# Kernel tuning notes

Measured on AMD Instinct MI355X. Metric: run time of the kernel, lower is better.

Reference implementation:

```python
import jax, jax.numpy as jnp
import numpy as np
from jax import lax

B, C_IN, C_OUT, KK, KS = 8, 32, 64, 4, 3
D, H, W = 32, 64, 64
PAD = 1

def setup_inputs() -> dict:
    key = jax.random.key(0)
    ks = jax.random.split(key, 12)
    s = 0.02
    return {
        "x": jax.random.normal(ks[0], (B, C_IN, D, H, W), jnp.float32),
        # K candidate conv kernels and biases
        "weight": jax.random.normal(ks[1], (KK, C_OUT, C_IN, KS, KS, KS), jnp.float32) * s,
        "cbias": jnp.zeros((KK, C_OUT), jnp.float32),
        "temperature": jnp.float32(34.0),
        # attention key path: BN(affine, eval-mode) -> GELU -> 1x1 conv (linear)
        "bn1_g": jnp.ones((C_IN,), jnp.float32),
        "bn1_b": jnp.zeros((C_IN,), jnp.float32),
        "w1": jax.random.normal(ks[2], (C_IN, C_IN), jnp.float32) * s,
        "b1": jnp.zeros((C_IN,), jnp.float32),
        "bn2_g": jnp.ones((C_IN,), jnp.float32),
        "bn2_b": jnp.zeros((C_IN,), jnp.float32),
        "w2": jax.random.normal(ks[3], (C_IN, C_IN), jnp.float32) * s,
        "b2": jnp.zeros((C_IN,), jnp.float32),
        "bn3_g": jnp.ones((C_IN,), jnp.float32),
        "bn3_b": jnp.zeros((C_IN,), jnp.float32),
        "w3": jax.random.normal(ks[4], (KK, C_IN), jnp.float32) * s,
        "b3": jnp.zeros((KK,), jnp.float32),
    }

def _attention(p, temperature, bn1_g, bn1_b, w1, b1, bn2_g, bn2_b, w2, b2, bn3_g, bn3_b, w3, b3):
    # p: [B, C] pooled features. 1x1x1 convs on 1x1x1 maps == linear layers.
    gelu = lambda t: jax.nn.gelu(t, approximate=False)  # torch nn.GELU default is erf
    a = gelu(p * bn1_g + bn1_b)          # BN (eval: rm=0, rv=1) + GELU
    a = a @ w1.T + b1
    a = gelu(a * bn2_g + bn2_b)
    a = a @ w2.T + b2
    a = a + p                            # ResidualLayer (plain add)
    a = a * bn3_g + bn3_b
    logits = a @ w3.T + b3               # [B, K]
    return jax.nn.softmax(logits / temperature, axis=1)

def reference(x, weight, cbias, temperature, bn1_g, bn1_b, w1, b1,
              bn2_g, bn2_b, w2, b2, bn3_g, bn3_b, w3, b3):
    # x: [B, C_in, D, H, W]
    p = x.mean(axis=(2, 3, 4))  # AdaptiveAvgPool3d(1)
    attn = _attention(p, temperature, bn1_g, bn1_b, w1, b1,
                      bn2_g, bn2_b, w2, b2, bn3_g, bn3_b, w3, b3)  # [B, K]
    # per-sample aggregated kernels / bias
    agg_w = jnp.einsum('bk,koidhw->boidhw', attn, weight)  # [B, O, I, k, k, k]
    agg_b = attn @ cbias                                    # [B, O]
    # grouped-conv trick (groups=B) == per-sample conv3d -> vmap over batch
    def conv1(xi, wi):
        return lax.conv_general_dilated(
            xi[None], wi, window_strides=(1, 1, 1),
            padding=[(PAD, PAD)] * 3,
            dimension_numbers=('NCDHW', 'OIDHW', 'NCDHW'))[0]
    out = jax.vmap(conv1)(x, agg_w)  # [B, O, D, H, W]
    return out + agg_b[:, :, None, None, None]
```

## Files before the change

### kernel.cpp

```cpp
#include <hip/hip_runtime.h>
#include <hip/hip_bf16.h>
#include <math.h>

#define B_   8
#define CIN  32
#define COUT 64
#define KK_  4
#define DD   32
#define HH   64
#define WW   64
#define HW   (HH*WW)
#define DHW  (DD*HH*WW)

typedef __attribute__((ext_vector_type(8)))  short bf16x8;
typedef __attribute__((ext_vector_type(16))) float f32x16;

__device__ __forceinline__ unsigned short f2bf(float f) {
    union { float f; unsigned int u; } v; v.f = f;
    return (unsigned short)((v.u + 0x7FFFu + ((v.u >> 16) & 1u)) >> 16);
}
__device__ __forceinline__ void gll16(const void* g, void* l) {
    __builtin_amdgcn_global_load_lds(
        (const __attribute__((address_space(1))) void*)g,
        (__attribute__((address_space(3))) void*)l, 16, 0, 0);
}

__global__ __launch_bounds__(256) void transpose_kernel(const float* __restrict__ x,
                                                        unsigned short* __restrict__ xt,
                                                        float* __restrict__ pblk) {
    const int t = threadIdx.x;
    const int r = t >> 6, w = t & 63;
    const int hb = blockIdx.x;
    const int h = (hb << 2) + r;
    const int d = blockIdx.y, b = blockIdx.z;

    const float* xb = x + (size_t)b*CIN*DHW + (size_t)d*HW + (size_t)h*WW + w;
    float f[CIN];
    #pragma unroll
    for (int c = 0; c < CIN; ++c) f[c] = xb[(size_t)c * DHW];

    unsigned int packed[CIN/2];
    #pragma unroll
    for (int c2 = 0; c2 < CIN/2; ++c2) {
        unsigned int lo = f2bf(f[2*c2]);
        unsigned int hi = f2bf(f[2*c2+1]);
        packed[c2] = lo | (hi << 16);
    }
    char* row = (char*)xt + (size_t)((b*DD + d)*HH + h) * 4096;
    #pragma unroll
    for (int q = 0; q < 4; ++q) {
        uint4 v = make_uint4(packed[4*q], packed[4*q+1], packed[4*q+2], packed[4*q+3]);
        *(uint4*)(row + q*1024 + (((w << 4)) ^ (q << 4))) = v;
    }

    #pragma unroll
    for (int off = 32; off > 0; off >>= 1) {
        #pragma unroll
        for (int c = 0; c < CIN; ++c) f[c] += __shfl_xor(f[c], off);
    }
    __shared__ float ws4[4][CIN];
    if ((t & 63) < CIN) ws4[r][t & 63] = f[t & 63];
    __syncthreads();
    if (t < CIN)
        pblk[(size_t)((b*DD + d)*16 + hb)*CIN + t] =
            ws4[0][t] + ws4[1][t] + ws4[2][t] + ws4[3][t];
}

__device__ __forceinline__ float gelu_erf(float v) {
    return 0.5f * v * (1.f + erff(v * 0.70710678118654752f));
}

__global__ void attn_kernel(const float* __restrict__ pblk,
                            const float* __restrict__ temperature,
                            const float* __restrict__ bn1_g, const float* __restrict__ bn1_b,
                            const float* __restrict__ w1,    const float* __restrict__ b1,
                            const float* __restrict__ bn2_g, const float* __restrict__ bn2_b,
                            const float* __restrict__ w2,    const float* __restrict__ b2,
                            const float* __restrict__ bn3_g, const float* __restrict__ bn3_b,
                            const float* __restrict__ w3,    const float* __restrict__ b3,
                            const float* __restrict__ cbias,
                            float* __restrict__ attn_out, float* __restrict__ aggb_out) {
    __shared__ float A[B_][CIN], A2[B_][CIN];
    __shared__ float L[B_][KK_], ATT[B_][KK_];
    const int t = threadIdx.x;
    const int b = t >> 5, c = t & 31;

    float pv = 0.f;
    for (int i = 0; i < DD*16; ++i) pv += pblk[(size_t)(b*DD*16 + i)*CIN + c];
    pv *= (1.f / (float)DHW);

    A[b][c] = gelu_erf(pv * bn1_g[c] + bn1_b[c]);
    __syncthreads();

    float s = b1[c];
    for (int j = 0; j < CIN; ++j) s += A[b][j] * w1[c*CIN + j];
    A2[b][c] = gelu_erf(s * bn2_g[c] + bn2_b[c]);
    __syncthreads();

    float s2 = b2[c];
    for (int j = 0; j < CIN; ++j) s2 += A2[b][j] * w2[c*CIN + j];
    s2 += pv;
    s2 = s2 * bn3_g[c] + bn3_b[c];
    __syncthreads();
    A[b][c] = s2;
    __syncthreads();

    if (c < KK_) {
        float lv = b3[c];
        for (int j = 0; j < CIN; ++j) lv += A[b][j] * w3[c*CIN + j];
        L[b][c] = lv;
    }
    __syncthreads();

    const float T = temperature[0];
    if (c < KK_) {
        float m = fmaxf(fmaxf(L[b][0], L[b][1]), fmaxf(L[b][2], L[b][3]));
        float e = expf((L[b][c] - m) / T);
        float den = 0.f;
        for (int j = 0; j < KK_; ++j) den += expf((L[b][j] - m) / T);
        float av = e / den;
        ATT[b][c] = av;
        attn_out[b*KK_ + c] = av;
    }
    __syncthreads();

    for (int o = c; o < COUT; o += CIN) {
        float sb = 0.f;
        for (int k = 0; k < KK_; ++k) sb += ATT[b][k] * cbias[k*COUT + o];
        aggb_out[b*COUT + o] = sb;
    }
}

__global__ void aggw_kernel(const float* __restrict__ weight,
                            const float* __restrict__ attn,
                            unsigned short* __restrict__ wt) {
    const int idx = blockIdx.x * 256 + threadIdx.x;
    const int ci   = idx & 31;
    const int co   = (idx >> 5) & 63;
    int r          = idx >> 11;
    const int kpos = r % 27;
    const int b    = r / 27;
    float s = 0.f;
    #pragma unroll
    for (int k = 0; k < KK_; ++k)
        s += attn[b*KK_ + k] * weight[((k*COUT + co)*CIN + ci)*27 + kpos];
    wt[idx] = f2bf(s);
}

__global__ __launch_bounds__(512, 4) void conv_mfma(const unsigned short* __restrict__ xt,
                                                    const unsigned short* __restrict__ wt,
                                                    const float* __restrict__ aggb,
                                                    float* __restrict__ out) {
    __shared__ char smem[19 * 4096];
    const int t    = threadIdx.x;
    const int lane = t & 63;
    const int wid  = t >> 6;
    const int cv   = wid & 1;
    const int wv   = (wid >> 1) & 1;
    const int dv   = wid >> 2;
    const int lw   = lane & 31, lh = lane >> 5;

    const int id = blockIdx.x;
    const int b  = id & 7;
    const int h  = (id >> 3) & 63;
    const int d0 = ((id >> 9) & 7) << 2;

    const char* xb  = (const char*)xt + (size_t)(b*DD)*HH*4096;
    const char* wtb = (const char*)wt + (size_t)b * 27 * 4096;

    if (t < 256) *(uint4*)&smem[18*4096 + t*16] = make_uint4(0u,0u,0u,0u);

    auto stage_row = [&](int zo, int ho) {
        const int zd = d0 - 1 + zo, yh = h - 1 + ho;
        char* dst = smem + (size_t)((zo*3 + ho) << 12);
        if ((unsigned)zd < DD && (unsigned)yh < HH) {
            const char* src = xb + (size_t)(zd*HH + yh)*4096 + lane*16;
            #pragma unroll
            for (int q = 0; q < 4; ++q) gll16(src + (q << 10), dst + (q << 10));
        } else {
            #pragma unroll
            for (int q = 0; q < 4; ++q)
                *(uint4*)(dst + (q << 10) + lane*16) = make_uint4(0u,0u,0u,0u);
        }
    };
    for (int rid = wid; rid < 18; rid += 8)
        stage_row(rid / 3, rid % 3);
    __syncthreads();

    f32x16 acc[2];
    acc[0] = (f32x16){};
    acc[1] = (f32x16){};

    const int a_off = (cv << 11) + lw*64 + lh*16;
    const int o0 = lh, o1 = 2 + lh;
    const int z0 = 18*4096 + (o0 << 10) + (lw << 4);
    const int z1 = 18*4096 + (o1 << 10) + (lw << 4);

    #pragma unroll
    for (int kh = 0; kh < 3; ++kh) {
        bf16x8 av[2][3][2];
        #pragma unroll
        for (int kw2 = 0; kw2 < 2; ++kw2)
            #pragma unroll
            for (int kd = 0; kd < 3; ++kd) {
                const char* wk = wtb + (size_t)(((kd*3 + kh)*3 + kw2) << 12);
                av[kw2][kd][0] = *(const bf16x8*)(wk + a_off);
                av[kw2][kd][1] = *(const bf16x8*)(wk + 32 + a_off);
            }
        asm volatile("" ::: "memory");

        #pragma unroll
        for (int kw = 0; kw < 3; ++kw) {
            if (kw == 2) {
                #pragma unroll
                for (int kd = 0; kd < 3; ++kd) {
                    const char* wk = wtb + (size_t)(((kd*3 + kh)*3 + 2) << 12);
                    av[0][kd][0] = *(const bf16x8*)(wk + a_off);
                    av[0][kd][1] = *(const bf16x8*)(wk + 32 + a_off);
                }
                asm volatile("" ::: "memory");
            }
            const int ai = (kw == 2) ? 0 : kw;

            const int wp  = (wv << 5) + lw + kw - 1;
            const bool oob = ((unsigned)wp >= (unsigned)WW);
            const int wpc = oob ? 0 : wp;
            const int sw0 = (o0 << 10) + ((wpc << 4) ^ (o0 << 4));
            const int sw1 = (o1 << 10) + ((wpc << 4) ^ (o1 << 4));

            const int rb0 = (((dv << 1) + 0)*3 + kh) << 12;
            const int rb1 = (((dv << 1) + 1)*3 + kh) << 12;
            const int rb2 = (((dv << 1) + 2)*3 + kh) << 12;
            const int rb3 = (((dv << 1) + 3)*3 + kh) << 12;

            bf16x8 bA0 = *(const bf16x8*)&smem[oob ? z0 : rb0 + sw0];
            bf16x8 bA1 = *(const bf16x8*)&smem[oob ? z1 : rb0 + sw1];
            bf16x8 bB0 = *(const bf16x8*)&smem[oob ? z0 : rb1 + sw0];
            bf16x8 bB1 = *(const bf16x8*)&smem[oob ? z1 : rb1 + sw1];

            acc[0] = __builtin_amdgcn_mfma_f32_32x32x16_bf16(av[ai][0][0], bA0, acc[0], 0, 0, 0);
            acc[0] = __builtin_amdgcn_mfma_f32_32x32x16_bf16(av[ai][0][1], bA1, acc[0], 0, 0, 0);
            acc[1] = __builtin_amdgcn_mfma_f32_32x32x16_bf16(av[ai][0][0], bB0, acc[1], 0, 0, 0);
            acc[1] = __builtin_amdgcn_mfma_f32_32x32x16_bf16(av[ai][0][1], bB1, acc[1], 0, 0, 0);

            bf16x8 bC0 = *(const bf16x8*)&smem[oob ? z0 : rb2 + sw0];
            bf16x8 bC1 = *(const bf16x8*)&smem[oob ? z1 : rb2 + sw1];

            acc[0] = __builtin_amdgcn_mfma_f32_32x32x16_bf16(av[ai][1][0], bB0, acc[0], 0, 0, 0);
            acc[0] = __builtin_amdgcn_mfma_f32_32x32x16_bf16(av[ai][1][1], bB1, acc[0], 0, 0, 0);
            acc[1] = __builtin_amdgcn_mfma_f32_32x32x16_bf16(av[ai][1][0], bC0, acc[1], 0, 0, 0);
            acc[1] = __builtin_amdgcn_mfma_f32_32x32x16_bf16(av[ai][1][1], bC1, acc[1], 0, 0, 0);

            bf16x8 bD0 = *(const bf16x8*)&smem[oob ? z0 : rb3 + sw0];
            bf16x8 bD1 = *(const bf16x8*)&smem[oob ? z1 : rb3 + sw1];

            acc[0] = __builtin_amdgcn_mfma_f32_32x32x16_bf16(av[ai][2][0], bC0, acc[0], 0, 0, 0);
            acc[0] = __builtin_amdgcn_mfma_f32_32x32x16_bf16(av[ai][2][1], bC1, acc[0], 0, 0, 0);
            acc[1] = __builtin_amdgcn_mfma_f32_32x32x16_bf16(av[ai][2][0], bD0, acc[1], 0, 0, 0);
            acc[1] = __builtin_amdgcn_mfma_f32_32x32x16_bf16(av[ai][2][1], bD1, acc[1], 0, 0, 0);
        }
    }

    const float* ab = aggb + b*COUT;
    const int sp0 = h*WW + (wv << 5) + lw;
    #pragma unroll
    for (int reg = 0; reg < 16; ++reg) {
        const int co = (cv << 5) + (reg & 3) + ((reg >> 2) << 3) + (lh << 2);
        const float bb = ab[co];
        float* oc = out + ((size_t)(b*COUT + co))*DHW + sp0;
        #pragma unroll
        for (int r = 0; r < 2; ++r)
            oc[(size_t)(d0 + (dv << 1) + r)*HW] = acc[r][reg] + bb;
    }
}

extern "C" void kernel_launch(void* const* d_in, const int* in_sizes, int n_in,
                              void* d_out, int out_size, void* d_ws, size_t ws_size,
                              hipStream_t stream) {
    const float* x           = (const float*)d_in[0];
    const float* weight      = (const float*)d_in[1];
    const float* cbias       = (const float*)d_in[2];
    const float* temperature = (const float*)d_in[3];
    const float* bn1_g       = (const float*)d_in[4];
    const float* bn1_b       = (const float*)d_in[5];
    const float* w1          = (const float*)d_in[6];
    const float* b1          = (const float*)d_in[7];
    const float* bn2_g       = (const float*)d_in[8];
    const float* bn2_b       = (const float*)d_in[9];
    const float* w2          = (const float*)d_in[10];
    const float* b2          = (const float*)d_in[11];
    const float* bn3_g       = (const float*)d_in[12];
    const float* bn3_b       = (const float*)d_in[13];
    const float* w3          = (const float*)d_in[14];
    const float* b3          = (const float*)d_in[15];
    float* out = (float*)d_out;

    char* ws = (char*)d_ws;
    float*          attn = (float*)(ws + 1024);
    float*          aggb = (float*)(ws + 4096);
    float*          pblk = (float*)(ws + 65536);
    unsigned short* wt   = (unsigned short*)(ws + 622592);
    unsigned short* xt   = (unsigned short*)(ws + 1507328);

    transpose_kernel<<<dim3(HH/4, DD, B_), 256, 0, stream>>>(x, xt, pblk);
    attn_kernel<<<1, 256, 0, stream>>>(pblk, temperature,
                                       bn1_g, bn1_b, w1, b1,
                                       bn2_g, bn2_b, w2, b2,
                                       bn3_g, bn3_b, w3, b3,
                                       cbias, attn, aggb);
    aggw_kernel<<<(B_*27*COUT*CIN)/256, 256, 0, stream>>>(weight, attn, wt);
    conv_mfma<<<dim3(64*8*8), 512, 0, stream>>>(xt, wt, aggb, out);
}
```

Baseline: 203.6 us.

## Pipeline input-row staging per kh phase with partial vmcnt barriers

Each of six waves now stages one depth slab of three input rows, and the last two waves zero the padding region. The single full barrier is replaced by three phases: each waits only until its kh row has landed in LDS (vmcnt(8), then 4, then 0) before its MFMAs run, so compute on early rows overlaps the loads of later rows. Weight fragments are now loaded per kw instead of being held across kw, which cuts register pressure, and the MFMA blocks are wrapped in s_setprio. The hand-written waitcnt counts depend on the order in which loads are issued and complete, and on the compiler not reordering them, which makes the barrier logic fragile.

```diff
diff --git a/kernel.cpp b/kernel.cpp
--- a/kernel.cpp
+++ b/kernel.cpp
@@ -168,24 +168,28 @@
     const char* xb  = (const char*)xt + (size_t)(b*DD)*HH*4096;
     const char* wtb = (const char*)wt + (size_t)b * 27 * 4096;
 
-    if (t < 256) *(uint4*)&smem[18*4096 + t*16] = make_uint4(0u,0u,0u,0u);
-
-    auto stage_row = [&](int zo, int ho) {
-        const int zd = d0 - 1 + zo, yh = h - 1 + ho;
-        char* dst = smem + (size_t)((zo*3 + ho) << 12);
-        if ((unsigned)zd < DD && (unsigned)yh < HH) {
-            const char* src = xb + (size_t)(zd*HH + yh)*4096 + lane*16;
-            #pragma unroll
-            for (int q = 0; q < 4; ++q) gll16(src + (q << 10), dst + (q << 10));
-        } else {
-            #pragma unroll
-            for (int q = 0; q < 4; ++q)
-                *(uint4*)(dst + (q << 10) + lane*16) = make_uint4(0u,0u,0u,0u);
+    if (wid < 6) {
+        const int zo = wid;
+        const int zd = d0 - 1 + zo;
+        #pragma unroll
+        for (int ho = 0; ho < 3; ++ho) {
+            const int yh = h - 1 + ho;
+            char* dst = smem + (size_t)((zo*3 + ho) << 12);
+            if ((unsigned)zd < DD && (unsigned)yh < HH) {
+                const char* src = xb + (size_t)(zd*HH + yh)*4096 + lane*16;
+                #pragma unroll
+                for (int q = 0; q < 4; ++q) gll16(src + (q << 10), dst + (q << 10));
+            } else {
+                #pragma unroll
+                for (int q = 0; q < 4; ++q)
+                    *(uint4*)(dst + (q << 10) + lane*16) = make_uint4(0u,0u,0u,0u);
+            }
         }
-    };
-    for (int rid = wid; rid < 18; rid += 8)
-        stage_row(rid / 3, rid % 3);
-    __syncthreads();
+    } else {
+        const int tz = t - 384;
+        *(uint4*)&smem[18*4096 + tz*32]      = make_uint4(0u,0u,0u,0u);
+        *(uint4*)&smem[18*4096 + tz*32 + 16] = make_uint4(0u,0u,0u,0u);
+    }
 
     f32x16 acc[2];
     acc[0] = (f32x16){};
@@ -196,31 +200,18 @@
     const int z0 = 18*4096 + (o0 << 10) + (lw << 4);
     const int z1 = 18*4096 + (o1 << 10) + (lw << 4);
 
-    #pragma unroll
-    for (int kh = 0; kh < 3; ++kh) {
-        bf16x8 av[2][3][2];
-        #pragma unroll
-        for (int kw2 = 0; kw2 < 2; ++kw2)
-            #pragma unroll
-            for (int kd = 0; kd < 3; ++kd) {
-                const char* wk = wtb + (size_t)(((kd*3 + kh)*3 + kw2) << 12);
-                av[kw2][kd][0] = *(const bf16x8*)(wk + a_off);
-                av[kw2][kd][1] = *(const bf16x8*)(wk + 32 + a_off);
-            }
-        asm volatile("" ::: "memory");
-
+    auto phase = [&](int kh) {
         #pragma unroll
         for (int kw = 0; kw < 3; ++kw) {
-            if (kw == 2) {
-                #pragma unroll
-                for (int kd = 0; kd < 3; ++kd) {
-                    const char* wk = wtb + (size_t)(((kd*3 + kh)*3 + 2) << 12);
-                    av[0][kd][0] = *(const bf16x8*)(wk + a_off);
-                    av[0][kd][1] = *(const bf16x8*)(wk + 32 + a_off);
-                }
-                asm volatile("" ::: "memory");
-            }
-            const int ai = (kw == 2) ? 0 : kw;
+            const char* wk0 = wtb + (size_t)(((0*3 + kh)*3 + kw) << 12);
+            const char* wk1 = wtb + (size_t)(((1*3 + kh)*3 + kw) << 12);
+            const char* wk2 = wtb + (size_t)(((2*3 + kh)*3 + kw) << 12);
+            bf16x8 a00 = *(const bf16x8*)(wk0 + a_off);
+            bf16x8 a01 = *(const bf16x8*)(wk0 + 32 + a_off);
+            bf16x8 a10 = *(const bf16x8*)(wk1 + a_off);
+            bf16x8 a11 = *(const bf16x8*)(wk1 + 32 + a_off);
+            bf16x8 a20 = *(const bf16x8*)(wk2 + a_off);
+            bf16x8 a21 = *(const bf16x8*)(wk2 + 32 + a_off);
 
             const int wp  = (wv << 5) + lw + kw - 1;
             const bool oob = ((unsigned)wp >= (unsigned)WW);
@@ -237,29 +228,48 @@
             bf16x8 bA1 = *(const bf16x8*)&smem[oob ? z1 : rb0 + sw1];
             bf16x8 bB0 = *(const bf16x8*)&smem[oob ? z0 : rb1 + sw0];
             bf16x8 bB1 = *(const bf16x8*)&smem[oob ? z1 : rb1 + sw1];
-
-            acc[0] = __builtin_amdgcn_mfma_f32_32x32x16_bf16(av[ai][0][0], bA0, acc[0], 0, 0, 0);
-            acc[0] = __builtin_amdgcn_mfma_f32_32x32x16_bf16(av[ai][0][1], bA1, acc[0], 0, 0, 0);
-            acc[1] = __builtin_amdgcn_mfma_f32_32x32x16_bf16(av[ai][0][0], bB0, acc[1], 0, 0, 0);
-            acc[1] = __builtin_amdgcn_mfma_f32_32x32x16_bf16(av[ai][0][1], bB1, acc[1], 0, 0, 0);
-
             bf16x8 bC0 = *(const bf16x8*)&smem[oob ? z0 : rb2 + sw0];
             bf16x8 bC1 = *(const bf16x8*)&smem[oob ? z1 : rb2 + sw1];
-
-            acc[0] = __builtin_amdgcn_mfma_f32_32x32x16_bf16(av[ai][1][0], bB0, acc[0], 0, 0, 0);
-            acc[0] = __builtin_amdgcn_mfma_f32_32x32x16_bf16(av[ai][1][1], bB1, acc[0], 0, 0, 0);
-            acc[1] = __builtin_amdgcn_mfma_f32_32x32x16_bf16(av[ai][1][0], bC0, acc[1], 0, 0, 0);
-            acc[1] = __builtin_amdgcn_mfma_f32_32x32x16_bf16(av[ai][1][1], bC1, acc[1], 0, 0, 0);
-
             bf16x8 bD0 = *(const bf16x8*)&smem[oob ? z0 : rb3 + sw0];
             bf16x8 bD1 = *(const bf16x8*)&smem[oob ? z1 : rb3 + sw1];
 
-            acc[0] = __builtin_amdgcn_mfma_f32_32x32x16_bf16(av[ai][2][0], bC0, acc[0], 0, 0, 0);
-            acc[0] = __builtin_amdgcn_mfma_f32_32x32x16_bf16(av[ai][2][1], bC1, acc[0], 0, 0, 0);
-            acc[1] = __builtin_amdgcn_mfma_f32_32x32x16_bf16(av[ai][2][0], bD0, acc[1], 0, 0, 0);
-            acc[1] = __builtin_amdgcn_mfma_f32_32x32x16_bf16(av[ai][2][1], bD1, acc[1], 0, 0, 0);
+            __builtin_amdgcn_s_setprio(1);
+            acc[0] = __builtin_amdgcn_mfma_f32_32x32x16_bf16(a00, bA0, acc[0], 0, 0, 0);
+            acc[0] = __builtin_amdgcn_mfma_f32_32x32x16_bf16(a01, bA1, acc[0], 0, 0, 0);
+            acc[1] = __builtin_amdgcn_mfma_f32_32x32x16_bf16(a00, bB0, acc[1], 0, 0, 0);
+            acc[1] = __builtin_amdgcn_mfma_f32_32x32x16_bf16(a01, bB1, acc[1], 0, 0, 0);
+            acc[0] = __builtin_amdgcn_mfma_f32_32x32x16_bf16(a10, bB0, acc[0], 0, 0, 0);
+            acc[0] = __builtin_amdgcn_mfma_f32_32x32x16_bf16(a11, bB1, acc[0], 0, 0, 0);
+            acc[1] = __builtin_amdgcn_mfma_f32_32x32x16_bf16(a10, bC0, acc[1], 0, 0, 0);
+            acc[1] = __builtin_amdgcn_mfma_f32_32x32x16_bf16(a11, bC1, acc[1], 0, 0, 0);
+            acc[0] = __builtin_amdgcn_mfma_f32_32x32x16_bf16(a20, bC0, acc[0], 0, 0, 0);
+            acc[0] = __builtin_amdgcn_mfma_f32_32x32x16_bf16(a21, bC1, acc[0], 0, 0, 0);
+            acc[1] = __builtin_amdgcn_mfma_f32_32x32x16_bf16(a20, bD0, acc[1], 0, 0, 0);
+            acc[1] = __builtin_amdgcn_mfma_f32_32x32x16_bf16(a21, bD1, acc[1], 0, 0, 0);
+            __builtin_amdgcn_s_setprio(0);
         }
-    }
+    };
+
+    __builtin_amdgcn_sched_barrier(0);
+    asm volatile("s_waitcnt vmcnt(8) lgkmcnt(0)" ::: "memory");
+    __builtin_amdgcn_s_barrier();
+    __builtin_amdgcn_sched_barrier(0);
+
+    phase(0);
+
+    __builtin_amdgcn_sched_barrier(0);
+    asm volatile("s_waitcnt vmcnt(4) lgkmcnt(0)" ::: "memory");
+    __builtin_amdgcn_s_barrier();
+    __builtin_amdgcn_sched_barrier(0);
+
+    phase(1);
+
+    __builtin_amdgcn_sched_barrier(0);
+    asm volatile("s_waitcnt vmcnt(0) lgkmcnt(0)" ::: "memory");
+    __builtin_amdgcn_s_barrier();
+    __builtin_amdgcn_sched_barrier(0);
+
+    phase(2);
 
     const float* ab = aggb + b*COUT;
     const int sp0 = h*WW + (wv << 5) + lw;
```

After: 209.7 us. +3.0%, slower.

## Give each conv wave a larger register tile with fewer waves per block

Applied to the files above, without the earlier changes.

The conv kernel drops from 8 waves to 2 waves per block. Each wave now computes all 64 output channels for all 4 depth slices (8 accumulators instead of 2). This reuses each LDS B-fragment and weight fragment across more MFMAs and removes the redundant per-wave reloads. The cost is much higher register pressure and only 2 waves per block, with a launch bound of 1 block, so latency hiding may drop. The zero row is also filled by fewer threads.

```diff
diff --git a/kernel.cpp b/kernel.cpp
--- a/kernel.cpp
+++ b/kernel.cpp
@@ -147,17 +147,14 @@
     wt[idx] = f2bf(s);
 }
 
-__global__ __launch_bounds__(512, 4) void conv_mfma(const unsigned short* __restrict__ xt,
+__global__ __launch_bounds__(128, 1) void conv_mfma(const unsigned short* __restrict__ xt,
                                                     const unsigned short* __restrict__ wt,
                                                     const float* __restrict__ aggb,
                                                     float* __restrict__ out) {
     __shared__ char smem[19 * 4096];
     const int t    = threadIdx.x;
     const int lane = t & 63;
-    const int wid  = t >> 6;
-    const int cv   = wid & 1;
-    const int wv   = (wid >> 1) & 1;
-    const int dv   = wid >> 2;
+    const int wv   = t >> 6;
     const int lw   = lane & 31, lh = lane >> 5;
 
     const int id = blockIdx.x;
@@ -168,11 +165,13 @@
     const char* xb  = (const char*)xt + (size_t)(b*DD)*HH*4096;
     const char* wtb = (const char*)wt + (size_t)b * 27 * 4096;
 
-    if (t < 256) *(uint4*)&smem[18*4096 + t*16] = make_uint4(0u,0u,0u,0u);
-
-    auto stage_row = [&](int zo, int ho) {
-        const int zd = d0 - 1 + zo, yh = h - 1 + ho;
-        char* dst = smem + (size_t)((zo*3 + ho) << 12);
+    *(uint4*)&smem[18*4096 + t*32]      = make_uint4(0u,0u,0u,0u);
+    *(uint4*)&smem[18*4096 + t*32 + 16] = make_uint4(0u,0u,0u,0u);
+
+    for (int rid = wv; rid < 18; rid += 2) {
+        const int j = rid / 3, ho = rid % 3;
+        const int zd = d0 - 1 + j, yh = h - 1 + ho;
+        char* dst = smem + (size_t)(rid << 12);
         if ((unsigned)zd < DD && (unsigned)yh < HH) {
             const char* src = xb + (size_t)(zd*HH + yh)*4096 + lane*16;
             #pragma unroll
@@ -182,95 +181,76 @@
             for (int q = 0; q < 4; ++q)
                 *(uint4*)(dst + (q << 10) + lane*16) = make_uint4(0u,0u,0u,0u);
         }
-    };
-    for (int rid = wid; rid < 18; rid += 8)
-        stage_row(rid / 3, rid % 3);
-    __syncthreads();
-
-    f32x16 acc[2];
-    acc[0] = (f32x16){};
-    acc[1] = (f32x16){};
-
-    const int a_off = (cv << 11) + lw*64 + lh*16;
+    }
+    __syncthreads();
+
+    f32x16 acc[2][4];
+    #pragma unroll
+    for (int cb = 0; cb < 2; ++cb)
+        #pragma unroll
+        for (int r = 0; r < 4; ++r)
+            acc[cb][r] = (f32x16){};
+
+    const int a_off = lw*64 + lh*16;
     const int o0 = lh, o1 = 2 + lh;
-    const int z0 = 18*4096 + (o0 << 10) + (lw << 4);
-    const int z1 = 18*4096 + (o1 << 10) + (lw << 4);
 
     #pragma unroll
     for (int kh = 0; kh < 3; ++kh) {
-        bf16x8 av[2][3][2];
-        #pragma unroll
-        for (int kw2 = 0; kw2 < 2; ++kw2)
+        #pragma unroll
+        for (int kw = 0; kw < 3; ++kw) {
+            bf16x8 av[3][2][2];
             #pragma unroll
             for (int kd = 0; kd < 3; ++kd) {
-                const char* wk = wtb + (size_t)(((kd*3 + kh)*3 + kw2) << 12);
-                av[kw2][kd][0] = *(const bf16x8*)(wk + a_off);
-                av[kw2][kd][1] = *(const bf16x8*)(wk + 32 + a_off);
+                const char* wk = wtb + (size_t)(((kd*3 + kh)*3 + kw) << 12);
+                av[kd][0][0] = *(const bf16x8*)(wk + a_off);
+                av[kd][0][1] = *(const bf16x8*)(wk + 32 + a_off);
+                av[kd][1][0] = *(const bf16x8*)(wk + 2048 + a_off);
+                av[kd][1][1] = *(const bf16x8*)(wk + 2048 + 32 + a_off);
             }
-        asm volatile("" ::: "memory");
-
-        #pragma unroll
-        for (int kw = 0; kw < 3; ++kw) {
-            if (kw == 2) {
-                #pragma unroll
-                for (int kd = 0; kd < 3; ++kd) {
-                    const char* wk = wtb + (size_t)(((kd*3 + kh)*3 + 2) << 12);
-                    av[0][kd][0] = *(const bf16x8*)(wk + a_off);
-                    av[0][kd][1] = *(const bf16x8*)(wk + 32 + a_off);
-                }
-                asm volatile("" ::: "memory");
-            }
-            const int ai = (kw == 2) ? 0 : kw;
 
             const int wp  = (wv << 5) + lw + kw - 1;
             const bool oob = ((unsigned)wp >= (unsigned)WW);
-            const int wpc = oob ? 0 : wp;
+            const int wpc = oob ? lw : wp;
             const int sw0 = (o0 << 10) + ((wpc << 4) ^ (o0 << 4));
             const int sw1 = (o1 << 10) + ((wpc << 4) ^ (o1 << 4));
-
-            const int rb0 = (((dv << 1) + 0)*3 + kh) << 12;
-            const int rb1 = (((dv << 1) + 1)*3 + kh) << 12;
-            const int rb2 = (((dv << 1) + 2)*3 + kh) << 12;
-            const int rb3 = (((dv << 1) + 3)*3 + kh) << 12;
-
-            bf16x8 bA0 = *(const bf16x8*)&smem[oob ? z0 : rb0 + sw0];
-            bf16x8 bA1 = *(const bf16x8*)&smem[oob ? z1 : rb0 + sw1];
-            bf16x8 bB0 = *(const bf16x8*)&smem[oob ? z0 : rb1 + sw0];
-            bf16x8 bB1 = *(const bf16x8*)&smem[oob ? z1 : rb1 + sw1];
-
-            acc[0] = __builtin_amdgcn_mfma_f32_32x32x16_bf16(av[ai][0][0], bA0, acc[0], 0, 0, 0);
-            acc[0] = __builtin_amdgcn_mfma_f32_32x32x16_bf16(av[ai][0][1], bA1, acc[0], 0, 0, 0);
-            acc[1] = __builtin_amdgcn_mfma_f32_32x32x16_bf16(av[ai][0][0], bB0, acc[1], 0, 0, 0);
-            acc[1] = __builtin_amdgcn_mfma_f32_32x32x16_bf16(av[ai][0][1], bB1, acc[1], 0, 0, 0);
-
-            bf16x8 bC0 = *(const bf16x8*)&smem[oob ? z0 : rb2 + sw0];
-            bf16x8 bC1 = *(const bf16x8*)&smem[oob ? z1 : rb2 + sw1];
-
-            acc[0] = __builtin_amdgcn_mfma_f32_32x32x16_bf16(av[ai][1][0], bB0, acc[0], 0, 0, 0);
-            acc[0] = __builtin_amdgcn_mfma_f32_32x32x16_bf16(av[ai][1][1], bB1, acc[0], 0, 0, 0);
-            acc[1] = __builtin_amdgcn_mfma_f32_32x32x16_bf16(av[ai][1][0], bC0, acc[1], 0, 0, 0);
-            acc[1] = __builtin_amdgcn_mfma_f32_32x32x16_bf16(av[ai][1][1], bC1, acc[1], 0, 0, 0);
-
-            bf16x8 bD0 = *(const bf16x8*)&smem[oob ? z0 : rb3 + sw0];
-            bf16x8 bD1 = *(const bf16x8*)&smem[oob ? z1 : rb3 + sw1];
-
-            acc[0] = __builtin_amdgcn_mfma_f32_32x32x16_bf16(av[ai][2][0], bC0, acc[0], 0, 0, 0);
-            acc[0] = __builtin_amdgcn_mfma_f32_32x32x16_bf16(av[ai][2][1], bC1, acc[0], 0, 0, 0);
-            acc[1] = __builtin_amdgcn_mfma_f32_32x32x16_bf16(av[ai][2][0], bD0, acc[1], 0, 0, 0);
-            acc[1] = __builtin_amdgcn_mfma_f32_32x32x16_bf16(av[ai][2][1], bD1, acc[1], 0, 0, 0);
+            const int zb  = oob ? 18*4096 : -1;
+
+            bf16x8 bc[6][2];
+            #pragma unroll
+            for (int j = 0; j < 6; ++j) {
+                const int rb = (j*3 + kh) << 12;
+                const int base = (zb >= 0) ? zb : rb;
+                bc[j][0] = *(const bf16x8*)&smem[base + sw0];
+                bc[j][1] = *(const bf16x8*)&smem[base + sw1];
+            }
+
+            #pragma unroll
+            for (int kd = 0; kd < 3; ++kd) {
+                #pragma unroll
+                for (int r = 0; r < 4; ++r) {
+                    const int j = r + kd;
+                    acc[0][r] = __builtin_amdgcn_mfma_f32_32x32x16_bf16(av[kd][0][0], bc[j][0], acc[0][r], 0, 0, 0);
+                    acc[0][r] = __builtin_amdgcn_mfma_f32_32x32x16_bf16(av[kd][0][1], bc[j][1], acc[0][r], 0, 0, 0);
+                    acc[1][r] = __builtin_amdgcn_mfma_f32_32x32x16_bf16(av[kd][1][0], bc[j][0], acc[1][r], 0, 0, 0);
+                    acc[1][r] = __builtin_amdgcn_mfma_f32_32x32x16_bf16(av[kd][1][1], bc[j][1], acc[1][r], 0, 0, 0);
+                }
+            }
         }
     }
 
     const float* ab = aggb + b*COUT;
     const int sp0 = h*WW + (wv << 5) + lw;
     #pragma unroll
-    for (int reg = 0; reg < 16; ++reg) {
-        const int co = (cv << 5) + (reg & 3) + ((reg >> 2) << 3) + (lh << 2);
-        const float bb = ab[co];
-        float* oc = out + ((size_t)(b*COUT + co))*DHW + sp0;
-        #pragma unroll
-        for (int r = 0; r < 2; ++r)
-            oc[(size_t)(d0 + (dv << 1) + r)*HW] = acc[r][reg] + bb;
+    for (int cb = 0; cb < 2; ++cb) {
+        #pragma unroll
+        for (int reg = 0; reg < 16; ++reg) {
+            const int co = (cb << 5) + (reg & 3) + ((reg >> 2) << 3) + (lh << 2);
+            const float bb = ab[co];
+            float* oc = out + ((size_t)(b*COUT + co))*DHW + sp0;
+            #pragma unroll
+            for (int r = 0; r < 4; ++r)
+                oc[(size_t)(d0 + r)*HW] = acc[cb][r][reg] + bb;
+        }
     }
 }
 
@@ -309,5 +289,5 @@
                                        bn3_g, bn3_b, w3, b3,
                                        cbias, attn, aggb);
     aggw_kernel<<<(B_*27*COUT*CIN)/256, 256, 0, stream>>>(weight, attn, wt);
-    conv_mfma<<<dim3(64*8*8), 512, 0, stream>>>(xt, wt, aggb, out);
-}
+    conv_mfma<<<dim3(64*8*8), 128, 0, stream>>>(xt, wt, aggb, out);
+}
```

Measured after the change: 213.4 us. 4.8% more time.
